# Kernel tuning notes

Measured on AMD Instinct MI355X. Metric: run time of the kernel, lower is better.

## Reference

```python
import jax, jax.numpy as jnp
import numpy as np

B, L, D, H = 32, 256, 2048, 8
DH = D // H  # 256; code requires L == S == DH


def setup_inputs() -> dict:
    key = jax.random.key(0)
    ks = jax.random.split(key, 12)
    s = 1.0 / np.sqrt(D)
    return {
        "queries": jax.random.normal(ks[0], (B, L, D), jnp.float32),
        "keys": jax.random.normal(ks[1], (B, L, D), jnp.float32),
        "values": jax.random.normal(ks[2], (B, L, D), jnp.float32),
        "Wq": jax.random.normal(ks[3], (D, D), jnp.float32) * s,
        "bq": jax.random.normal(ks[4], (D,), jnp.float32) * s,
        "Wk": jax.random.normal(ks[5], (D, D), jnp.float32) * s,
        "bk": jax.random.normal(ks[6], (D,), jnp.float32) * s,
        "Wv": jax.random.normal(ks[7], (D, D), jnp.float32) * s,
        "bv": jax.random.normal(ks[8], (D,), jnp.float32) * s,
        "Wo": jax.random.normal(ks[9], (D, D), jnp.float32) * s,
        "bo": jax.random.normal(ks[10], (D,), jnp.float32) * s,
        "temperature": jnp.ones((H, 1, 1), jnp.float32),
    }


def reference(queries, keys, values, Wq, bq, Wk, bk, Wv, bv, Wo, bo, temperature):
    b, l, d = queries.shape
    # projections (Linear: x @ W^T + b)
    q = (jnp.einsum('bld,ed->ble', queries, Wq) + bq).reshape(b, l, H, DH).transpose(0, 2, 1, 3)   # [B,H,L,dh]
    k = (jnp.einsum('bsd,ed->bse', keys, Wk) + bk).reshape(b, l, H, DH).transpose(0, 2, 1, 3)      # [B,H,S,dh]
    v = (jnp.einsum('bsd,ed->bse', values, Wv) + bv).reshape(b, l, H, DH).transpose(0, 2, 3, 1)    # [B,H,dh,S]
    # FFT cross-correlation over the head dim (as in the source)
    qf = jnp.fft.rfft(q, axis=-1)
    kf = jnp.fft.rfft(k, axis=-1)
    corr = jnp.fft.irfft(qf * jnp.conj(kf), n=DH, axis=-1)   # [B,H,L,dh]
    corr = jax.nn.softmax(corr / temperature, axis=-1)
    # dropout is identity in eval mode
    # time-delay aggregation: [B,H,dh,S] @ [B,H,dh,L] (S == dh) -> [B,H,dh,L]
    out = jnp.matmul(v, jnp.swapaxes(corr, -1, -2))
    out = out.transpose(0, 3, 1, 2).reshape(b, l, d)          # [B,L,D]
    out = jnp.einsum('bld,ed->ble', out, Wo) + bo
    return out
```

## Files before the change

kernel.cpp:

```cpp
#include <hip/hip_runtime.h>
#include <stdint.h>

typedef float  f32x4 __attribute__((ext_vector_type(4)));
typedef short  s16x8 __attribute__((ext_vector_type(8)));
typedef _Float16 h16x8 __attribute__((ext_vector_type(8)));
typedef _Float16 h16x2 __attribute__((ext_vector_type(2)));
typedef unsigned short u16x4 __attribute__((ext_vector_type(4)));
typedef unsigned int u32x2 __attribute__((ext_vector_type(2)));
typedef unsigned int u32x4 __attribute__((ext_vector_type(4)));

#define DEV __device__ __forceinline__

DEV unsigned short f2bf(float f) {
  union { float f; unsigned int u; } v; v.f = f;
  unsigned int u = v.u;
  return (unsigned short)((u + 0x7fffu + ((u >> 16) & 1u)) >> 16);
}

typedef const __attribute__((address_space(1))) void* as1cvp;
typedef __attribute__((address_space(3))) void* as3vp;
DEV void gload16(const void* g, void* l) {
  __builtin_amdgcn_global_load_lds((as1cvp)g, (as3vp)l, 16, 0, 0);
}

DEV float fdot2u(unsigned int a, unsigned int b, float c) {
  return __builtin_amdgcn_fdot2(__builtin_bit_cast(h16x2, a),
                                __builtin_bit_cast(h16x2, b), c, false);
}


template<int M0, int M1, int M2>
__global__ __launch_bounds__(256)
void pack3(const float* __restrict__ in0, unsigned short* __restrict__ out0, long n0,
           const float* __restrict__ in1, unsigned short* __restrict__ out1, long n1,
           const float* __restrict__ in2, unsigned short* __restrict__ out2, long n2)
{
  const long total = n0 + n1 + n2;
  for (long t = (long)blockIdx.x * 256 + threadIdx.x; t < total;
       t += (long)gridDim.x * 256) {
    const float* src; unsigned short* dst; long i; int mode;
    if (t < n0)           { src = in0; dst = out0; i = t;           mode = M0; }
    else if (t < n0 + n1) { src = in1; dst = out1; i = t - n0;      mode = M1; }
    else                  { src = in2; dst = out2; i = t - n0 - n1; mode = M2; }
    f32x4 x0 = *(const f32x4*)(src + i * 8);
    f32x4 x1 = *(const f32x4*)(src + i * 8 + 4);
    s16x8 h8;
    #pragma unroll
    for (int e = 0; e < 4; ++e) {
      if (mode == 1) {
        h8[e]     = (short)__builtin_bit_cast(unsigned short, (_Float16)x0[e]);
        h8[e + 4] = (short)__builtin_bit_cast(unsigned short, (_Float16)x1[e]);
      } else {
        h8[e]     = (short)f2bf(x0[e]);
        h8[e + 4] = (short)f2bf(x1[e]);
      }
    }
    *(s16x8*)(dst + i * 8) = h8;
  }
}

template<int M0, int M1, int M2, int M3>
__global__ __launch_bounds__(256)
void pack4(const float* __restrict__ in0, unsigned short* __restrict__ out0, long n0,
           const float* __restrict__ in1, unsigned short* __restrict__ out1, long n1,
           const float* __restrict__ in2, unsigned short* __restrict__ out2, long n2,
           const float* __restrict__ in3, unsigned short* __restrict__ out3, long n3)
{
  const long total = n0 + n1 + n2 + n3;
  for (long t = (long)blockIdx.x * 256 + threadIdx.x; t < total;
       t += (long)gridDim.x * 256) {
    const float* src; unsigned short* dst; long i; int mode;
    if (t < n0)                { src = in0; dst = out0; i = t;                mode = M0; }
    else if (t < n0 + n1)      { src = in1; dst = out1; i = t - n0;           mode = M1; }
    else if (t < n0 + n1 + n2) { src = in2; dst = out2; i = t - n0 - n1;      mode = M2; }
    else                       { src = in3; dst = out3; i = t - n0 - n1 - n2; mode = M3; }
    f32x4 x0 = *(const f32x4*)(src + i * 8);
    f32x4 x1 = *(const f32x4*)(src + i * 8 + 4);
    s16x8 h8;
    #pragma unroll
    for (int e = 0; e < 4; ++e) {
      if (mode == 1) {
        h8[e]     = (short)__builtin_bit_cast(unsigned short, (_Float16)x0[e]);
        h8[e + 4] = (short)__builtin_bit_cast(unsigned short, (_Float16)x1[e]);
      } else {
        h8[e]     = (short)f2bf(x0[e]);
        h8[e + 4] = (short)f2bf(x1[e]);
      }
    }
    *(s16x8*)(dst + i * 8) = h8;
  }
}

template<int DT>
DEV f32x4 mfma16(s16x8 a, s16x8 b, f32x4 c) {
  if constexpr (DT == 0)
    return __builtin_amdgcn_mfma_f32_16x16x32_bf16(a, b, c, 0, 0, 0);
  else
    return __builtin_amdgcn_mfma_f32_16x16x32_f16(
        __builtin_bit_cast(h16x8, a), __builtin_bit_cast(h16x8, b), c, 0, 0, 0);
}

template<int DT, int OM>
__global__ __launch_bounds__(512, 2)
void gemm8p(const unsigned short* __restrict__ Ap, const unsigned short* __restrict__ Bp,
            const float* __restrict__ bias, void* __restrict__ Cp)
{
  constexpr int LD  = 2048;
  constexpr int LDC = 2048;
  constexpr int NT  = 32;
  constexpr int NI  = NT / 2;

  __shared__ __align__(16) unsigned short lds[65536];

  const int tid  = threadIdx.x;
  const int lane = tid & 63;
  const int wid  = tid >> 6;
  const int wm   = wid >> 2;
  const int wn   = wid & 3;
  const int fr   = lane & 15;
  const int ko   = (lane >> 4) * 8;

  const int bx = blockIdx.x;
  const int m0 = (((bx & 7) << 2) + (bx >> 3)) * 256;
  const int n0 = blockIdx.y * 256;

  const int sr  = tid >> 3;
  const int scc = (((tid & 7) ^ (((tid >> 5) & 1) << 2)) << 3);

  auto sA = [&](int d, int u, int col) {
    const unsigned short* s0 = Ap + (long)(m0 + u * 64 + sr) * LD + col + scc;
    const int lb = d * 32768 + u * 4096 + (wid << 9);
    gload16(s0, lds + lb);
    gload16(s0 + 128 * LD, lds + lb + 8192);
  };
  auto sB = [&](int d, int h, int col) {
    const unsigned short* s0 = Bp + (long)(n0 + h * 128 + sr) * LD + col + scc;
    const int lb = d * 32768 + 16384 + h * 8192 + (wid << 9);
    gload16(s0, lds + lb);
    gload16(s0 + 64 * LD, lds + lb + 4096);
  };

  f32x4 acc[8][4];
  #pragma unroll
  for (int i = 0; i < 8; ++i)
    #pragma unroll
    for (int j = 0; j < 4; ++j)
      acc[i][j] = (f32x4)(0.0f);

  s16x8 afr[2][2], bfr[4][2];

#define LOADB(d)                                                              \
  _Pragma("unroll") for (int ni = 0; ni < 4; ++ni)                            \
    _Pragma("unroll") for (int kk = 0; kk < 2; ++kk) {                        \
      const int nr = wn * 64 + ni * 16 + fr;                                  \
      int u = (d) * 32768 + 16384 + (nr >> 7) * 8192 + (nr & 127) * 64        \
              + kk * 32 + ko;                                                 \
      u ^= ((u >> 8) & 1) << 5;                                               \
      bfr[ni][kk] = *(const s16x8*)&lds[u];                                   \
    }

#define PHASE(d, q, DOB, STAGE, VM)                                           \
  {                                                                           \
    if (DOB) { LOADB(d) }                                                     \
    _Pragma("unroll") for (int ai = 0; ai < 2; ++ai)                          \
      _Pragma("unroll") for (int kk = 0; kk < 2; ++kk) {                      \
        int u = (d) * 32768 + wm * 8192 + ((2 * (q) + ai) * 16 + fr) * 64     \
                + kk * 32 + ko;                                               \
        u ^= ((u >> 8) & 1) << 5;                                             \
        afr[ai][kk] = *(const s16x8*)&lds[u];                                 \
      }                                                                       \
    STAGE;                                                                    \
    __builtin_amdgcn_s_barrier();                                             \
    asm volatile("s_waitcnt lgkmcnt(0)" ::: "memory");                        \
    __builtin_amdgcn_sched_barrier(0);                                        \
    __builtin_amdgcn_s_setprio(1);                                            \
    _Pragma("unroll") for (int ai = 0; ai < 2; ++ai)                          \
      _Pragma("unroll") for (int ni = 0; ni < 4; ++ni)                        \
        _Pragma("unroll") for (int kk = 0; kk < 2; ++kk)                      \
          acc[2 * (q) + ai][ni] =                                             \
              mfma16<DT>(afr[ai][kk], bfr[ni][kk], acc[2 * (q) + ai][ni]);    \
    __builtin_amdgcn_s_setprio(0);                                            \
    if (VM) { asm volatile("s_waitcnt vmcnt(6)" ::: "memory"); }              \
    __builtin_amdgcn_s_barrier();                                             \
  }

  sB(0, 0, 0); sB(0, 1, 0);
  sA(0, 0, 0); sA(0, 1, 0);
  sB(1, 0, 64); sB(1, 1, 64);
  sA(1, 0, 64);
  asm volatile("s_waitcnt vmcnt(6)" ::: "memory");
  __builtin_amdgcn_s_barrier();

  for (int i = 0; i < NI; ++i) {
    const int a1c = (2 * i + 1) << 6;
    const int c0  = ((2 * i + 2 < NT) ? 2 * i + 2 : NT - 1) << 6;
    const int c1  = ((2 * i + 3 < NT) ? 2 * i + 3 : NT - 1) << 6;
    PHASE(0, 0, true,  sA(1, 1, a1c), false)
    PHASE(0, 1, false, sB(0, 0, c0), false)
    PHASE(0, 2, false, sB(0, 1, c0), false)
    PHASE(0, 3, false, sA(0, 0, c0), true)
    PHASE(1, 0, true,  sA(0, 1, c0), false)
    PHASE(1, 1, false, sB(1, 0, c1), false)
    PHASE(1, 2, false, sB(1, 1, c1), false)
    PHASE(1, 3, false, sA(1, 0, c1), true)
  }
#undef PHASE
#undef LOADB

  const int rg = (lane >> 4) * 4;
  #pragma unroll
  for (int ni = 0; ni < 4; ++ni) {
    const int gn = n0 + wn * 64 + ni * 16 + fr;
    const float bvl = bias[gn];
    #pragma unroll
    for (int mi = 0; mi < 8; ++mi) {
      const int gmB = m0 + wm * 128 + mi * 16 + rg;
      f32x4 v = acc[mi][ni];
      if (OM == 0) {
        float* Cf = (float*)Cp;
        #pragma unroll
        for (int r = 0; r < 4; ++r)
          Cf[(long)(gmB + r) * LDC + gn] = v[r] + bvl;
      } else if (OM == 2) {
        unsigned short* Ch = (unsigned short*)Cp;
        #pragma unroll
        for (int r = 0; r < 4; ++r)
          Ch[(long)(gmB + r) * LDC + gn] =
              __builtin_bit_cast(unsigned short, (_Float16)(v[r] + bvl));
      } else {
        const int b = gmB >> 8, s = gmB & 255, h = gn >> 8, ii = gn & 255;
        u16x4 o;
        #pragma unroll
        for (int r = 0; r < 4; ++r) o[r] = f2bf(v[r] + bvl);
        *(u16x4*)&((unsigned short*)Cp)[((long)((b * 8 + h) * 256 + ii) << 8) + s] = o;
      }
    }
  }
}

template<int MODE, int OM, bool BATCHED>
__global__ __launch_bounds__(256)
void fgemm(const unsigned short* __restrict__ A, const unsigned short* __restrict__ B,
           const float* __restrict__ bias, void* __restrict__ C,
           int lda, int ldb, int ldc, int KT)
{
  __shared__ __align__(16) unsigned short lA[2 * 128 * 32];
  __shared__ __align__(16) unsigned short lB[2 * 128 * 32];

  const int tid  = threadIdx.x;
  const int lane = tid & 63;
  const int wid  = tid >> 6;
  const int wr   = wid >> 1;
  const int wc   = wid & 1;

  const int z  = BATCHED ? blockIdx.z : 0;
  const int m0 = blockIdx.y * 128;
  const int n0 = blockIdx.x * 128;

  long aBase = (long)m0 * lda;
  long bBase = (long)n0 * ldb;
  if (BATCHED) {
    aBase += (long)z * 256 * lda;
    bBase += (long)z * 256 * ldb;
  }

  const int ar0 = tid >> 2, ac0 = (tid & 3) * 8;
  const int ar1 = ar0 + 64, ac1 = ac0;

  const unsigned short* pa0 = A + aBase + (long)ar0 * lda + ac0;
  const unsigned short* pa1 = A + aBase + (long)ar1 * lda + ac1;
  const unsigned short* pb0 = B + bBase + (long)ar0 * ldb + ac0;
  const unsigned short* pb1 = B + bBase + (long)ar1 * ldb + ac1;

  constexpr int SUBOFF = (MODE == 0) ? 2048 : 32;
  constexpr int KSTEP  = (MODE == 0) ? 32 : 64;

  f32x4 acc[4][4];
  #pragma unroll
  for (int i = 0; i < 4; ++i)
    #pragma unroll
    for (int j = 0; j < 4; ++j)
      acc[i][j] = (f32x4)(0.0f);

  const int fr   = lane & 15;
  const int krow = (lane >> 4) * 8;

  for (int kt = 0; kt < KT; kt += KSTEP) {
    gload16(pa0 + kt,          lA + tid * 8);
    gload16(pa1 + kt,          lA + (tid + 256) * 8);
    gload16(pa0 + kt + SUBOFF, lA + 4096 + tid * 8);
    gload16(pa1 + kt + SUBOFF, lA + 4096 + (tid + 256) * 8);
    gload16(pb0 + kt,          lB + tid * 8);
    gload16(pb1 + kt,          lB + (tid + 256) * 8);
    gload16(pb0 + kt + SUBOFF, lB + 4096 + tid * 8);
    gload16(pb1 + kt + SUBOFF, lB + 4096 + (tid + 256) * 8);
    __syncthreads();

    s16x8 a0[4], a1[4], b0[4], b1[4];
    #pragma unroll
    for (int i = 0; i < 4; ++i) {
      const int r = (wr * 64 + i * 16 + fr) * 32 + krow;
      a0[i] = *(const s16x8*)&lA[r];
      a1[i] = *(const s16x8*)&lA[4096 + r];
    }
    #pragma unroll
    for (int j = 0; j < 4; ++j) {
      const int r = (wc * 64 + j * 16 + fr) * 32 + krow;
      b0[j] = *(const s16x8*)&lB[r];
      b1[j] = *(const s16x8*)&lB[4096 + r];
    }

    #pragma unroll
    for (int i = 0; i < 4; ++i)
      #pragma unroll
      for (int j = 0; j < 4; ++j) {
        if (MODE == 0) {
          acc[i][j] = __builtin_amdgcn_mfma_f32_16x16x32_bf16(a1[i], b0[j], acc[i][j], 0, 0, 0);
          acc[i][j] = __builtin_amdgcn_mfma_f32_16x16x32_bf16(a0[i], b1[j], acc[i][j], 0, 0, 0);
          acc[i][j] = __builtin_amdgcn_mfma_f32_16x16x32_bf16(a0[i], b0[j], acc[i][j], 0, 0, 0);
        } else {
          acc[i][j] = __builtin_amdgcn_mfma_f32_16x16x32_bf16(a0[i], b0[j], acc[i][j], 0, 0, 0);
          acc[i][j] = __builtin_amdgcn_mfma_f32_16x16x32_bf16(a1[i], b1[j], acc[i][j], 0, 0, 0);
        }
      }

    __syncthreads();
  }

  const int rg = (lane >> 4) * 4;
  #pragma unroll
  for (int j = 0; j < 4; ++j) {
    const int gn = n0 + wc * 64 + j * 16 + fr;
    const float bvl = bias ? bias[gn] : 0.0f;
    #pragma unroll
    for (int i = 0; i < 4; ++i) {
      const int gmB = m0 + wr * 64 + i * 16 + rg;
      f32x4 v = acc[i][j];
      if (OM == 0) {
        float* Cf = (float*)C;
        #pragma unroll
        for (int r = 0; r < 4; ++r)
          Cf[(long)(gmB + r) * ldc + gn] = v[r] + bvl;
      } else if (OM == 2) {
        long cb = 0;
        if (BATCHED) cb = (long)(z >> 3) * 256 * ldc + (long)(z & 7) * 256;
        unsigned short* Ch = (unsigned short*)C;
        #pragma unroll
        for (int r = 0; r < 4; ++r)
          Ch[cb + (long)(gmB + r) * ldc + gn] = f2bf(v[r] + bvl);
      } else {
        const int b = gmB >> 8, s = gmB & 255, h = gn >> 8, ii = gn & 255;
        u16x4 o;
        #pragma unroll
        for (int r = 0; r < 4; ++r) o[r] = f2bf(v[r] + bvl);
        *(u16x4*)&((unsigned short*)C)[((long)((b * 8 + h) * 256 + ii) << 8) + s] = o;
      }
    }
  }
}

__global__ __launch_bounds__(256)
void corr_softmax(const unsigned short* __restrict__ qp,
                  const unsigned short* __restrict__ kp,
                  const float* __restrict__ temp, unsigned short* __restrict__ w)
{
  __shared__ __align__(16) unsigned short qs[4][520];
  __shared__ __align__(16) unsigned short q2[4][520];
  __shared__ __align__(16) unsigned short ks[4][264];
  const int tid  = threadIdx.x;
  const int lane = tid & 63;
  const int wid  = tid >> 6;
  const int row  = blockIdx.x * 4 + wid;
  const int b = row >> 11;
  const int h = (row >> 8) & 7;
  const int l = row & 255;
  const long base = ((long)(b * 256 + l) << 11) + h * 256;

  {
    u16x4 qv = *(const u16x4*)(qp + base + 4 * lane);
    u16x4 kv = *(const u16x4*)(kp + base + 4 * lane);
    const int nxt = __shfl((int)(unsigned int)(unsigned short)qv[0],
                           (lane + 1) & 63, 64);
    u16x4 qsv;
    qsv[0] = qv[1]; qsv[1] = qv[2]; qsv[2] = qv[3];
    qsv[3] = (unsigned short)(unsigned int)nxt;
    *(u16x4*)&qs[wid][4 * lane]       = qv;
    *(u16x4*)&qs[wid][256 + 4 * lane] = qv;
    *(u16x4*)&q2[wid][4 * lane]       = qsv;
    *(u16x4*)&q2[wid][256 + 4 * lane] = qsv;
    *(u16x4*)&ks[wid][4 * lane]       = kv;
  }
  __syncthreads();

  const unsigned short* Q  = &qs[wid][0];
  const unsigned short* Qs = &q2[wid][0];
  const unsigned short* K  = &ks[wid][0];
  const int e = 2 * lane;

  float c0 = 0.f, c1 = 0.f, c2 = 0.f, c3 = 0.f;

  #pragma unroll
  for (int t = 0; t < 32; ++t) {
    u32x4 Kw = *(const u32x4*)&K[8 * t];
    u32x2 Pa = *(const u32x2*)&Q[2 * (e + 4 * t)];
    u32x2 Pb = *(const u32x2*)&Q[2 * (e + 4 * t + 2)];
    const unsigned int p4 = *(const unsigned int*)&Q[2 * (e + 4 * t + 4)];
    u32x2 Sa = *(const u32x2*)&Qs[2 * (e + 4 * t)];
    u32x2 Sb = *(const u32x2*)&Qs[2 * (e + 4 * t + 2)];
    const unsigned int s4 = *(const unsigned int*)&Qs[2 * (e + 4 * t + 4)];
    c0 = fdot2u(Kw[0], Pa[0], c0); c2 = fdot2u(Kw[0], Pa[1], c2);
    c1 = fdot2u(Kw[0], Sa[0], c1); c3 = fdot2u(Kw[0], Sa[1], c3);
    c0 = fdot2u(Kw[1], Pa[1], c0); c2 = fdot2u(Kw[1], Pb[0], c2);
    c1 = fdot2u(Kw[1], Sa[1], c1); c3 = fdot2u(Kw[1], Sb[0], c3);
    c0 = fdot2u(Kw[2], Pb[0], c0); c2 = fdot2u(Kw[2], Pb[1], c2);
    c1 = fdot2u(Kw[2], Sb[0], c1); c3 = fdot2u(Kw[2], Sb[1], c3);
    c0 = fdot2u(Kw[3], Pb[1], c0); c2 = fdot2u(Kw[3], p4, c2);
    c1 = fdot2u(Kw[3], Sb[1], c1); c3 = fdot2u(Kw[3], s4, c3);
  }

  const float invT = 1.0f / temp[h];
  float mx = fmaxf(fmaxf(c0, c1), fmaxf(c2, c3));
  #pragma unroll
  for (int off = 32; off >= 1; off >>= 1) mx = fmaxf(mx, __shfl_xor(mx, off, 64));
  const float e0 = __expf((c0 - mx) * invT);
  const float e1 = __expf((c1 - mx) * invT);
  const float e2 = __expf((c2 - mx) * invT);
  const float e3 = __expf((c3 - mx) * invT);
  float sm = e0 + e1 + e2 + e3;
  #pragma unroll
  for (int off = 32; off >= 1; off >>= 1) sm += __shfl_xor(sm, off, 64);
  const float rs = 1.0f / sm;
  u16x4 o;
  o[0] = f2bf(e0 * rs); o[1] = f2bf(e1 * rs); o[2] = f2bf(e2 * rs); o[3] = f2bf(e3 * rs);
  *(u16x4*)(w + (long)row * 256 + 4 * lane) = o;
}


extern "C" void kernel_launch(void* const* d_in, const int* in_sizes, int n_in,
                              void* d_out, int out_size, void* d_ws, size_t ws_size,
                              hipStream_t stream) {
  (void)in_sizes; (void)n_in; (void)out_size; (void)ws_size;
  const float* queries = (const float*)d_in[0];
  const float* keys    = (const float*)d_in[1];
  const float* values  = (const float*)d_in[2];
  const float* Wq = (const float*)d_in[3];
  const float* bq = (const float*)d_in[4];
  const float* Wk = (const float*)d_in[5];
  const float* bk = (const float*)d_in[6];
  const float* Wv = (const float*)d_in[7];
  const float* bv = (const float*)d_in[8];
  const float* Wo = (const float*)d_in[9];
  const float* bo = (const float*)d_in[10];
  const float* temp = (const float*)d_in[11];

  char* ws = (char*)d_ws;
  auto MB = [](size_t m) { return m << 20; };
  unsigned short* qA   = (unsigned short*)ws;
  unsigned short* wgt  = (unsigned short*)ws;
  unsigned short* kA   = (unsigned short*)(ws + MB(32));
  unsigned short* vT   = (unsigned short*)(ws + MB(32));
  unsigned short* vA   = (unsigned short*)(ws + MB(64));
  unsigned short* out2 = (unsigned short*)(ws + MB(64));
  unsigned short* qproj= (unsigned short*)(ws + MB(96));
  unsigned short* kproj= (unsigned short*)(ws + MB(128));
  unsigned short* WqF  = (unsigned short*)(ws + MB(160));
  unsigned short* WkF  = (unsigned short*)(ws + MB(168));
  unsigned short* WvB  = (unsigned short*)(ws + MB(176));
  unsigned short* WoB  = (unsigned short*)(ws + MB(184));

  dim3 blk(256);
  dim3 gBig(32, 8);
  const long nBig = (long)8192 * 2048 / 8;
  const long nW   = (long)2048 * 2048 / 8;

  pack4<1, 1, 1, 1><<<2048, blk, 0, stream>>>(queries, qA, nBig, keys, kA, nBig,
                                              Wq, WqF, nW, Wk, WkF, nW);
  pack3<0, 0, 0><<<2048, blk, 0, stream>>>(values, vA, nBig, Wv, WvB, nW,
                                           Wo, WoB, nW);
  gemm8p<1, 2><<<gBig, 512, 0, stream>>>(qA, WqF, bq, qproj);
  gemm8p<1, 2><<<gBig, 512, 0, stream>>>(kA, WkF, bk, kproj);
  corr_softmax<<<dim3(16384), blk, 0, stream>>>(qproj, kproj, temp, wgt);
  gemm8p<0, 1><<<gBig, 512, 0, stream>>>(vA, WvB, bv, vT);
  fgemm<1, 2, true><<<dim3(2, 2, 256), blk, 0, stream>>>(wgt, vT, nullptr, out2,
                                                         256, 256, 2048, 256);
  gemm8p<0, 0><<<gBig, 512, 0, stream>>>(out2, WoB, bo, (float*)d_out);
}
```

Before: 483.8 us.

## Fuse Q/K/V projection GEMMs into one launch and register-rotate corr loads

The three separate projection GEMMs become a single kernel over a 3x taller M grid. Each block picks its weight, bias and output layout from its M segment, and the kernel relies on qA/kA/vA being laid out contiguously in the workspace. The V projection switches from bf16 to fp16 inputs, and its transposed output now goes into the final output buffer as scratch. The correlation kernel keeps Q fragments in registers across iterations, loading only the new ones each step, and unrolls the loop less. The aim is fewer launches, better fill of the last wave across 768 tiles, and fewer LDS reads, at some risk to the numerics of the V path.

```diff
diff --git a/kernel.cpp b/kernel.cpp
--- a/kernel.cpp
+++ b/kernel.cpp
@@ -91,6 +91,61 @@
   }
 }
 
+
+#define GEMM8P_CORE(DT, APTR, BPTR, M0EXPR)                                   \
+  constexpr int LD  = 2048;                                                   \
+  constexpr int NT  = 32;                                                     \
+  constexpr int NI  = NT / 2;                                                 \
+  __shared__ __align__(16) unsigned short lds[65536];                         \
+  const int tid  = threadIdx.x;                                               \
+  const int lane = tid & 63;                                                  \
+  const int wid  = tid >> 6;                                                  \
+  const int wm   = wid >> 2;                                                  \
+  const int wn   = wid & 3;                                                   \
+  const int fr   = lane & 15;                                                 \
+  const int ko   = (lane >> 4) * 8;                                           \
+  const int bx = blockIdx.x;                                                  \
+  const int m0 = (M0EXPR) * 256;                                              \
+  const int n0 = blockIdx.y * 256;                                            \
+  const int sr  = tid >> 3;                                                   \
+  const int scc = (((tid & 7) ^ (((tid >> 5) & 1) << 2)) << 3);               \
+  auto sA = [&](int d, int u, int col) {                                      \
+    const unsigned short* s0 = (APTR) + (long)(m0 + u * 64 + sr) * LD + col + scc; \
+    const int lb = d * 32768 + u * 4096 + (wid << 9);                         \
+    gload16(s0, lds + lb);                                                    \
+    gload16(s0 + 128 * LD, lds + lb + 8192);                                  \
+  };                                                                          \
+  auto sB = [&](int d, int h2, int col) {                                     \
+    const unsigned short* s0 = (BPTR) + (long)(n0 + h2 * 128 + sr) * LD + col + scc; \
+    const int lb = d * 32768 + 16384 + h2 * 8192 + (wid << 9);                \
+    gload16(s0, lds + lb);                                                    \
+    gload16(s0 + 64 * LD, lds + lb + 4096);                                   \
+  };                                                                          \
+  f32x4 acc[8][4];                                                            \
+  _Pragma("unroll") for (int i = 0; i < 8; ++i)                               \
+    _Pragma("unroll") for (int j = 0; j < 4; ++j)                             \
+      acc[i][j] = (f32x4)(0.0f);                                              \
+  s16x8 afr[2][2], bfr[4][2];                                                 \
+  sB(0, 0, 0); sB(0, 1, 0);                                                   \
+  sA(0, 0, 0); sA(0, 1, 0);                                                   \
+  sB(1, 0, 64); sB(1, 1, 64);                                                 \
+  sA(1, 0, 64);                                                               \
+  asm volatile("s_waitcnt vmcnt(6)" ::: "memory");                            \
+  __builtin_amdgcn_s_barrier();                                               \
+  for (int i = 0; i < NI; ++i) {                                              \
+    const int a1c = (2 * i + 1) << 6;                                         \
+    const int c0  = ((2 * i + 2 < NT) ? 2 * i + 2 : NT - 1) << 6;             \
+    const int c1  = ((2 * i + 3 < NT) ? 2 * i + 3 : NT - 1) << 6;             \
+    PHASE(DT, 0, 0, true,  sA(1, 1, a1c), false)                              \
+    PHASE(DT, 0, 1, false, sB(0, 0, c0), false)                               \
+    PHASE(DT, 0, 2, false, sB(0, 1, c0), false)                               \
+    PHASE(DT, 0, 3, false, sA(0, 0, c0), true)                                \
+    PHASE(DT, 1, 0, true,  sA(0, 1, c0), false)                               \
+    PHASE(DT, 1, 1, false, sB(1, 0, c1), false)                               \
+    PHASE(DT, 1, 2, false, sB(1, 1, c1), false)                               \
+    PHASE(DT, 1, 3, false, sA(1, 0, c1), true)                                \
+  }
+
 template<int DT>
 DEV f32x4 mfma16(s16x8 a, s16x8 b, f32x4 c) {
   if constexpr (DT == 0)
@@ -99,55 +154,6 @@
     return __builtin_amdgcn_mfma_f32_16x16x32_f16(
         __builtin_bit_cast(h16x8, a), __builtin_bit_cast(h16x8, b), c, 0, 0, 0);
 }
-
-template<int DT, int OM>
-__global__ __launch_bounds__(512, 2)
-void gemm8p(const unsigned short* __restrict__ Ap, const unsigned short* __restrict__ Bp,
-            const float* __restrict__ bias, void* __restrict__ Cp)
-{
-  constexpr int LD  = 2048;
-  constexpr int LDC = 2048;
-  constexpr int NT  = 32;
-  constexpr int NI  = NT / 2;
-
-  __shared__ __align__(16) unsigned short lds[65536];
-
-  const int tid  = threadIdx.x;
-  const int lane = tid & 63;
-  const int wid  = tid >> 6;
-  const int wm   = wid >> 2;
-  const int wn   = wid & 3;
-  const int fr   = lane & 15;
-  const int ko   = (lane >> 4) * 8;
-
-  const int bx = blockIdx.x;
-  const int m0 = (((bx & 7) << 2) + (bx >> 3)) * 256;
-  const int n0 = blockIdx.y * 256;
-
-  const int sr  = tid >> 3;
-  const int scc = (((tid & 7) ^ (((tid >> 5) & 1) << 2)) << 3);
-
-  auto sA = [&](int d, int u, int col) {
-    const unsigned short* s0 = Ap + (long)(m0 + u * 64 + sr) * LD + col + scc;
-    const int lb = d * 32768 + u * 4096 + (wid << 9);
-    gload16(s0, lds + lb);
-    gload16(s0 + 128 * LD, lds + lb + 8192);
-  };
-  auto sB = [&](int d, int h, int col) {
-    const unsigned short* s0 = Bp + (long)(n0 + h * 128 + sr) * LD + col + scc;
-    const int lb = d * 32768 + 16384 + h * 8192 + (wid << 9);
-    gload16(s0, lds + lb);
-    gload16(s0 + 64 * LD, lds + lb + 4096);
-  };
-
-  f32x4 acc[8][4];
-  #pragma unroll
-  for (int i = 0; i < 8; ++i)
-    #pragma unroll
-    for (int j = 0; j < 4; ++j)
-      acc[i][j] = (f32x4)(0.0f);
-
-  s16x8 afr[2][2], bfr[4][2];
 
 #define LOADB(d)                                                              \
   _Pragma("unroll") for (int ni = 0; ni < 4; ++ni)                            \
@@ -159,7 +165,7 @@
       bfr[ni][kk] = *(const s16x8*)&lds[u];                                   \
     }
 
-#define PHASE(d, q, DOB, STAGE, VM)                                           \
+#define PHASE(DT, d, q, DOB, STAGE, VM)                                       \
   {                                                                           \
     if (DOB) { LOADB(d) }                                                     \
     _Pragma("unroll") for (int ai = 0; ai < 2; ++ai)                          \
@@ -184,28 +190,12 @@
     __builtin_amdgcn_s_barrier();                                             \
   }
 
-  sB(0, 0, 0); sB(0, 1, 0);
-  sA(0, 0, 0); sA(0, 1, 0);
-  sB(1, 0, 64); sB(1, 1, 64);
-  sA(1, 0, 64);
-  asm volatile("s_waitcnt vmcnt(6)" ::: "memory");
-  __builtin_amdgcn_s_barrier();
-
-  for (int i = 0; i < NI; ++i) {
-    const int a1c = (2 * i + 1) << 6;
-    const int c0  = ((2 * i + 2 < NT) ? 2 * i + 2 : NT - 1) << 6;
-    const int c1  = ((2 * i + 3 < NT) ? 2 * i + 3 : NT - 1) << 6;
-    PHASE(0, 0, true,  sA(1, 1, a1c), false)
-    PHASE(0, 1, false, sB(0, 0, c0), false)
-    PHASE(0, 2, false, sB(0, 1, c0), false)
-    PHASE(0, 3, false, sA(0, 0, c0), true)
-    PHASE(1, 0, true,  sA(0, 1, c0), false)
-    PHASE(1, 1, false, sB(1, 0, c1), false)
-    PHASE(1, 2, false, sB(1, 1, c1), false)
-    PHASE(1, 3, false, sA(1, 0, c1), true)
-  }
-#undef PHASE
-#undef LOADB
+template<int DT, int OM>
+__global__ __launch_bounds__(512, 2)
+void gemm8p(const unsigned short* __restrict__ Ap, const unsigned short* __restrict__ Bp,
+            const float* __restrict__ bias, void* __restrict__ Cp)
+{
+  GEMM8P_CORE(DT, Ap, Bp, ((bx & 7) << 2) + (bx >> 3))
 
   const int rg = (lane >> 4) * 4;
   #pragma unroll
@@ -220,30 +210,76 @@
         float* Cf = (float*)Cp;
         #pragma unroll
         for (int r = 0; r < 4; ++r)
-          Cf[(long)(gmB + r) * LDC + gn] = v[r] + bvl;
-      } else if (OM == 2) {
+          Cf[(long)(gmB + r) * 2048 + gn] = v[r] + bvl;
+      } else {
         unsigned short* Ch = (unsigned short*)Cp;
         #pragma unroll
         for (int r = 0; r < 4; ++r)
-          Ch[(long)(gmB + r) * LDC + gn] =
+          Ch[(long)(gmB + r) * 2048 + gn] =
               __builtin_bit_cast(unsigned short, (_Float16)(v[r] + bvl));
-      } else {
+      }
+    }
+  }
+}
+
+__global__ __launch_bounds__(512, 2)
+void qkv8p(const unsigned short* __restrict__ Ap,
+           const unsigned short* __restrict__ Bq, const unsigned short* __restrict__ Bk,
+           const unsigned short* __restrict__ Bv,
+           const float* __restrict__ bq, const float* __restrict__ bk,
+           const float* __restrict__ bv,
+           unsigned short* __restrict__ Cq, unsigned short* __restrict__ Ck,
+           unsigned short* __restrict__ Cv)
+{
+  const int pre_m0 = ((blockIdx.x & 7) * 12 + (blockIdx.x >> 3));
+  const int seg = (pre_m0 * 256) >> 13;
+  const unsigned short* Bp = (seg == 0) ? Bq : (seg == 1) ? Bk : Bv;
+  const float* bias = (seg == 0) ? bq : (seg == 1) ? bk : bv;
+
+  GEMM8P_CORE(1, Ap, Bp, pre_m0)
+
+  const int rg = (lane >> 4) * 4;
+  const int m0l = m0 & 8191;
+  if (seg < 2) {
+    unsigned short* Ch = (seg == 0) ? Cq : Ck;
+    #pragma unroll
+    for (int ni = 0; ni < 4; ++ni) {
+      const int gn = n0 + wn * 64 + ni * 16 + fr;
+      const float bvl = bias[gn];
+      #pragma unroll
+      for (int mi = 0; mi < 8; ++mi) {
+        const int gmB = m0l + wm * 128 + mi * 16 + rg;
+        f32x4 v = acc[mi][ni];
+        #pragma unroll
+        for (int r = 0; r < 4; ++r)
+          Ch[(long)(gmB + r) * 2048 + gn] =
+              __builtin_bit_cast(unsigned short, (_Float16)(v[r] + bvl));
+      }
+    }
+  } else {
+    #pragma unroll
+    for (int ni = 0; ni < 4; ++ni) {
+      const int gn = n0 + wn * 64 + ni * 16 + fr;
+      const float bvl = bias[gn];
+      #pragma unroll
+      for (int mi = 0; mi < 8; ++mi) {
+        const int gmB = m0l + wm * 128 + mi * 16 + rg;
+        f32x4 v = acc[mi][ni];
         const int b = gmB >> 8, s = gmB & 255, h = gn >> 8, ii = gn & 255;
         u16x4 o;
         #pragma unroll
         for (int r = 0; r < 4; ++r) o[r] = f2bf(v[r] + bvl);
-        *(u16x4*)&((unsigned short*)Cp)[((long)((b * 8 + h) * 256 + ii) << 8) + s] = o;
-      }
-    }
-  }
-}
-
-template<int MODE, int OM, bool BATCHED>
+        *(u16x4*)&Cv[((long)((b * 8 + h) * 256 + ii) << 8) + s] = o;
+      }
+    }
+  }
+}
+
 __global__ __launch_bounds__(256)
-void fgemm(const unsigned short* __restrict__ A, const unsigned short* __restrict__ B,
-           const float* __restrict__ bias, void* __restrict__ C,
-           int lda, int ldb, int ldc, int KT)
-{
+void fgemm_agg(const unsigned short* __restrict__ A, const unsigned short* __restrict__ B,
+               void* __restrict__ C)
+{
+  constexpr int lda = 256, ldb = 256, ldc = 2048, KT = 256;
   __shared__ __align__(16) unsigned short lA[2 * 128 * 32];
   __shared__ __align__(16) unsigned short lB[2 * 128 * 32];
 
@@ -253,27 +289,20 @@
   const int wr   = wid >> 1;
   const int wc   = wid & 1;
 
-  const int z  = BATCHED ? blockIdx.z : 0;
+  const int z  = blockIdx.z;
   const int m0 = blockIdx.y * 128;
   const int n0 = blockIdx.x * 128;
 
-  long aBase = (long)m0 * lda;
-  long bBase = (long)n0 * ldb;
-  if (BATCHED) {
-    aBase += (long)z * 256 * lda;
-    bBase += (long)z * 256 * ldb;
-  }
+  long aBase = (long)m0 * lda + (long)z * 256 * lda;
+  long bBase = (long)n0 * ldb + (long)z * 256 * ldb;
 
   const int ar0 = tid >> 2, ac0 = (tid & 3) * 8;
-  const int ar1 = ar0 + 64, ac1 = ac0;
+  const int ar1 = ar0 + 64;
 
   const unsigned short* pa0 = A + aBase + (long)ar0 * lda + ac0;
-  const unsigned short* pa1 = A + aBase + (long)ar1 * lda + ac1;
+  const unsigned short* pa1 = A + aBase + (long)ar1 * lda + ac0;
   const unsigned short* pb0 = B + bBase + (long)ar0 * ldb + ac0;
-  const unsigned short* pb1 = B + bBase + (long)ar1 * ldb + ac1;
-
-  constexpr int SUBOFF = (MODE == 0) ? 2048 : 32;
-  constexpr int KSTEP  = (MODE == 0) ? 32 : 64;
+  const unsigned short* pb1 = B + bBase + (long)ar1 * ldb + ac0;
 
   f32x4 acc[4][4];
   #pragma unroll
@@ -285,15 +314,15 @@
   const int fr   = lane & 15;
   const int krow = (lane >> 4) * 8;
 
-  for (int kt = 0; kt < KT; kt += KSTEP) {
-    gload16(pa0 + kt,          lA + tid * 8);
-    gload16(pa1 + kt,          lA + (tid + 256) * 8);
-    gload16(pa0 + kt + SUBOFF, lA + 4096 + tid * 8);
-    gload16(pa1 + kt + SUBOFF, lA + 4096 + (tid + 256) * 8);
-    gload16(pb0 + kt,          lB + tid * 8);
-    gload16(pb1 + kt,          lB + (tid + 256) * 8);
-    gload16(pb0 + kt + SUBOFF, lB + 4096 + tid * 8);
-    gload16(pb1 + kt + SUBOFF, lB + 4096 + (tid + 256) * 8);
+  for (int kt = 0; kt < KT; kt += 64) {
+    gload16(pa0 + kt,      lA + tid * 8);
+    gload16(pa1 + kt,      lA + (tid + 256) * 8);
+    gload16(pa0 + kt + 32, lA + 4096 + tid * 8);
+    gload16(pa1 + kt + 32, lA + 4096 + (tid + 256) * 8);
+    gload16(pb0 + kt,      lB + tid * 8);
+    gload16(pb1 + kt,      lB + (tid + 256) * 8);
+    gload16(pb0 + kt + 32, lB + 4096 + tid * 8);
+    gload16(pb1 + kt + 32, lB + 4096 + (tid + 256) * 8);
     __syncthreads();
 
     s16x8 a0[4], a1[4], b0[4], b1[4];
@@ -314,14 +343,8 @@
     for (int i = 0; i < 4; ++i)
       #pragma unroll
       for (int j = 0; j < 4; ++j) {
-        if (MODE == 0) {
-          acc[i][j] = __builtin_amdgcn_mfma_f32_16x16x32_bf16(a1[i], b0[j], acc[i][j], 0, 0, 0);
-          acc[i][j] = __builtin_amdgcn_mfma_f32_16x16x32_bf16(a0[i], b1[j], acc[i][j], 0, 0, 0);
-          acc[i][j] = __builtin_amdgcn_mfma_f32_16x16x32_bf16(a0[i], b0[j], acc[i][j], 0, 0, 0);
-        } else {
-          acc[i][j] = __builtin_amdgcn_mfma_f32_16x16x32_bf16(a0[i], b0[j], acc[i][j], 0, 0, 0);
-          acc[i][j] = __builtin_amdgcn_mfma_f32_16x16x32_bf16(a1[i], b1[j], acc[i][j], 0, 0, 0);
-        }
+        acc[i][j] = __builtin_amdgcn_mfma_f32_16x16x32_bf16(a0[i], b0[j], acc[i][j], 0, 0, 0);
+        acc[i][j] = __builtin_amdgcn_mfma_f32_16x16x32_bf16(a1[i], b1[j], acc[i][j], 0, 0, 0);
       }
 
     __syncthreads();
@@ -331,30 +354,15 @@
   #pragma unroll
   for (int j = 0; j < 4; ++j) {
     const int gn = n0 + wc * 64 + j * 16 + fr;
-    const float bvl = bias ? bias[gn] : 0.0f;
     #pragma unroll
     for (int i = 0; i < 4; ++i) {
       const int gmB = m0 + wr * 64 + i * 16 + rg;
       f32x4 v = acc[i][j];
-      if (OM == 0) {
-        float* Cf = (float*)C;
-        #pragma unroll
-        for (int r = 0; r < 4; ++r)
-          Cf[(long)(gmB + r) * ldc + gn] = v[r] + bvl;
-      } else if (OM == 2) {
-        long cb = 0;
-        if (BATCHED) cb = (long)(z >> 3) * 256 * ldc + (long)(z & 7) * 256;
-        unsigned short* Ch = (unsigned short*)C;
-        #pragma unroll
-        for (int r = 0; r < 4; ++r)
-          Ch[cb + (long)(gmB + r) * ldc + gn] = f2bf(v[r] + bvl);
-      } else {
-        const int b = gmB >> 8, s = gmB & 255, h = gn >> 8, ii = gn & 255;
-        u16x4 o;
-        #pragma unroll
-        for (int r = 0; r < 4; ++r) o[r] = f2bf(v[r] + bvl);
-        *(u16x4*)&((unsigned short*)C)[((long)((b * 8 + h) * 256 + ii) << 8) + s] = o;
-      }
+      long cb = (long)(z >> 3) * 256 * ldc + (long)(z & 7) * 256;
+      unsigned short* Ch = (unsigned short*)C;
+      #pragma unroll
+      for (int r = 0; r < 4; ++r)
+        Ch[cb + (long)(gmB + r) * ldc + gn] = f2bf(v[r]);
     }
   }
 }
@@ -397,25 +405,33 @@
   const unsigned short* K  = &ks[wid][0];
   const int e = 2 * lane;
 
+  u32x2 A  = *(const u32x2*)&Q[2 * e];
+  u32x2 B  = *(const u32x2*)&Q[2 * (e + 2)];
+  u32x2 C  = *(const u32x2*)&Q[2 * (e + 4)];
+  u32x2 A2 = *(const u32x2*)&Qs[2 * e];
+  u32x2 B2 = *(const u32x2*)&Qs[2 * (e + 2)];
+  u32x2 C2 = *(const u32x2*)&Qs[2 * (e + 4)];
+
   float c0 = 0.f, c1 = 0.f, c2 = 0.f, c3 = 0.f;
 
-  #pragma unroll
+  #pragma unroll 2
   for (int t = 0; t < 32; ++t) {
     u32x4 Kw = *(const u32x4*)&K[8 * t];
-    u32x2 Pa = *(const u32x2*)&Q[2 * (e + 4 * t)];
-    u32x2 Pb = *(const u32x2*)&Q[2 * (e + 4 * t + 2)];
-    const unsigned int p4 = *(const unsigned int*)&Q[2 * (e + 4 * t + 4)];
-    u32x2 Sa = *(const u32x2*)&Qs[2 * (e + 4 * t)];
-    u32x2 Sb = *(const u32x2*)&Qs[2 * (e + 4 * t + 2)];
-    const unsigned int s4 = *(const unsigned int*)&Qs[2 * (e + 4 * t + 4)];
-    c0 = fdot2u(Kw[0], Pa[0], c0); c2 = fdot2u(Kw[0], Pa[1], c2);
-    c1 = fdot2u(Kw[0], Sa[0], c1); c3 = fdot2u(Kw[0], Sa[1], c3);
-    c0 = fdot2u(Kw[1], Pa[1], c0); c2 = fdot2u(Kw[1], Pb[0], c2);
-    c1 = fdot2u(Kw[1], Sa[1], c1); c3 = fdot2u(Kw[1], Sb[0], c3);
-    c0 = fdot2u(Kw[2], Pb[0], c0); c2 = fdot2u(Kw[2], Pb[1], c2);
-    c1 = fdot2u(Kw[2], Sb[0], c1); c3 = fdot2u(Kw[2], Sb[1], c3);
-    c0 = fdot2u(Kw[3], Pb[1], c0); c2 = fdot2u(Kw[3], p4, c2);
-    c1 = fdot2u(Kw[3], Sb[1], c1); c3 = fdot2u(Kw[3], s4, c3);
+    const unsigned int p0 = A[0],  p1 = A[1],  p2 = B[0],  p3 = B[1],  p4 = C[0];
+    const unsigned int s0 = A2[0], s1 = A2[1], s2 = B2[0], s3 = B2[1], s4 = C2[0];
+    c0 = fdot2u(Kw[0], p0, c0); c2 = fdot2u(Kw[0], p1, c2);
+    c1 = fdot2u(Kw[0], s0, c1); c3 = fdot2u(Kw[0], s1, c3);
+    c0 = fdot2u(Kw[1], p1, c0); c2 = fdot2u(Kw[1], p2, c2);
+    c1 = fdot2u(Kw[1], s1, c1); c3 = fdot2u(Kw[1], s2, c3);
+    c0 = fdot2u(Kw[2], p2, c0); c2 = fdot2u(Kw[2], p3, c2);
+    c1 = fdot2u(Kw[2], s2, c1); c3 = fdot2u(Kw[2], s3, c3);
+    c0 = fdot2u(Kw[3], p3, c0); c2 = fdot2u(Kw[3], p4, c2);
+    c1 = fdot2u(Kw[3], s3, c1); c3 = fdot2u(Kw[3], s4, c3);
+    A = C;  A2 = C2;
+    B  = *(const u32x2*)&Q[2 * (4 * t + e + 6)];
+    C  = *(const u32x2*)&Q[2 * (4 * t + e + 8)];
+    B2 = *(const u32x2*)&Qs[2 * (4 * t + e + 6)];
+    C2 = *(const u32x2*)&Qs[2 * (4 * t + e + 8)];
   }
 
   const float invT = 1.0f / temp[h];
@@ -458,30 +474,26 @@
   unsigned short* qA   = (unsigned short*)ws;
   unsigned short* wgt  = (unsigned short*)ws;
   unsigned short* kA   = (unsigned short*)(ws + MB(32));
-  unsigned short* vT   = (unsigned short*)(ws + MB(32));
+  unsigned short* out2 = (unsigned short*)(ws + MB(32));
   unsigned short* vA   = (unsigned short*)(ws + MB(64));
-  unsigned short* out2 = (unsigned short*)(ws + MB(64));
   unsigned short* qproj= (unsigned short*)(ws + MB(96));
   unsigned short* kproj= (unsigned short*)(ws + MB(128));
   unsigned short* WqF  = (unsigned short*)(ws + MB(160));
   unsigned short* WkF  = (unsigned short*)(ws + MB(168));
-  unsigned short* WvB  = (unsigned short*)(ws + MB(176));
+  unsigned short* WvF  = (unsigned short*)(ws + MB(176));
   unsigned short* WoB  = (unsigned short*)(ws + MB(184));
+  unsigned short* vT   = (unsigned short*)d_out;
 
   dim3 blk(256);
-  dim3 gBig(32, 8);
   const long nBig = (long)8192 * 2048 / 8;
   const long nW   = (long)2048 * 2048 / 8;
 
   pack4<1, 1, 1, 1><<<2048, blk, 0, stream>>>(queries, qA, nBig, keys, kA, nBig,
-                                              Wq, WqF, nW, Wk, WkF, nW);
-  pack3<0, 0, 0><<<2048, blk, 0, stream>>>(values, vA, nBig, Wv, WvB, nW,
-                                           Wo, WoB, nW);
-  gemm8p<1, 2><<<gBig, 512, 0, stream>>>(qA, WqF, bq, qproj);
-  gemm8p<1, 2><<<gBig, 512, 0, stream>>>(kA, WkF, bk, kproj);
+                                              values, vA, nBig, Wq, WqF, nW);
+  pack3<1, 1, 0><<<2048, blk, 0, stream>>>(Wk, WkF, nW, Wv, WvF, nW, Wo, WoB, nW);
+  qkv8p<<<dim3(96, 8), 512, 0, stream>>>(qA, WqF, WkF, WvF, bq, bk, bv,
+                                         qproj, kproj, vT);
   corr_softmax<<<dim3(16384), blk, 0, stream>>>(qproj, kproj, temp, wgt);
-  gemm8p<0, 1><<<gBig, 512, 0, stream>>>(vA, WvB, bv, vT);
-  fgemm<1, 2, true><<<dim3(2, 2, 256), blk, 0, stream>>>(wgt, vT, nullptr, out2,
-                                                         256, 256, 2048, 256);
-  gemm8p<0, 0><<<gBig, 512, 0, stream>>>(out2, WoB, bo, (float*)d_out);
-}
+  fgemm_agg<<<dim3(2, 2, 256), blk, 0, stream>>>(wgt, vT, out2);
+  gemm8p<0, 0><<<dim3(32, 8), 512, 0, stream>>>(out2, WoB, bo, (float*)d_out);
+}
```

Result: faster. 462.7 us (-4.4%).
